# Kernel tuning notes

Hardware: AMD Instinct MI355X
Metric: run time of the kernel (lower is better)

## Reference

```python
import jax, jax.numpy as jnp
import numpy as np

B, DIM = 64, 1024

def setup_inputs() -> dict:
    key = jax.random.key(0)
    ks = jax.random.split(key, 16)
    d = {
        'x': jax.random.normal(ks[0], (B, DIM), jnp.float32),
        'C': jax.random.normal(ks[1], (B, DIM, DIM), jnp.float32) * 0.02,
        'n': jax.random.normal(ks[2], (B, DIM), jnp.float32),
        'm': jax.random.normal(ks[3], (B, DIM), jnp.float32),
    }
    s = 1.0 / np.sqrt(DIM)
    names = ['q', 'k', 'v', 'i', 'f', 'o']
    for j, nm in enumerate(names):
        d['W' + nm] = jax.random.uniform(ks[4 + 2 * j], (DIM, DIM), jnp.float32, -s, s)
        d['b' + nm] = jax.random.uniform(ks[5 + 2 * j], (DIM,), jnp.float32, -s, s)
    return d

def _lin(x, W, b):
    # torch nn.Linear: x @ W.T + b
    return x @ W.T + b

def reference(x, C, n, m, Wq, bq, Wk, bk, Wv, bv, Wi, bi, Wf, bf, Wo, bo):
    q = _lin(x, Wq, bq)                      # [B, D]
    k = _lin(x, Wk, bk) / jnp.sqrt(jnp.float32(DIM))
    v = _lin(x, Wv, bv)
    i_t = _lin(x, Wi, bi)
    f_t = _lin(x, Wf, bf)
    m_new = jnp.maximum(f_t + m, i_t)        # [B, D]
    i = jnp.exp(i_t - m_new)                 # [B, D]
    f = jnp.exp(f_t + m - m_new)             # [B, D]
    # rank-1 covariance update: C_new[b,r,c] = f[b,r]*C[b,r,c] + i[b,r]*v[b,r]*k[b,c]
    C_new = f[:, :, None] * C + (i * v)[:, :, None] * k[:, None, :]
    n_new = f * n + i * k
    h = jax.nn.sigmoid(_lin(x, Wo, bo)) * jnp.einsum('brc,bc->br', C_new, q)
    return (h, C_new, n_new, m_new)
```

## Files before the change

kernel.cpp:

```cpp
#include <hip/hip_runtime.h>
#include <math.h>

#define BATCH 64
#define DIM 1024
#define NROW (BATCH * DIM)
#define OFF_H 0
#define OFF_C 65536
#define OFF_N (65536 + 67108864)
#define OFF_M (OFF_N + 65536)

typedef float f4 __attribute__((ext_vector_type(4)));


__global__ __launch_bounds__(256) void gemm6(
    const float* __restrict__ x,
    const float* __restrict__ Wq, const float* __restrict__ bq,
    const float* __restrict__ Wk, const float* __restrict__ bk,
    const float* __restrict__ Wv, const float* __restrict__ bv,
    const float* __restrict__ Wi, const float* __restrict__ bi,
    const float* __restrict__ Wf, const float* __restrict__ bf,
    const float* __restrict__ Wo, const float* __restrict__ bo,
    float* __restrict__ pre)
{
    __shared__ float xs[64][64];
    __shared__ float wl[64][17];

    const int bx = blockIdx.x;
    const int g = bx >> 6;
    const int j0 = (bx & 63) * 16;
    const float* W; const float* bias;
    switch (g) {
        case 0: W = Wq; bias = bq; break;
        case 1: W = Wk; bias = bk; break;
        case 2: W = Wv; bias = bv; break;
        case 3: W = Wi; bias = bi; break;
        case 4: W = Wf; bias = bf; break;
        default: W = Wo; bias = bo; break;
    }

    const int tid = threadIdx.x;
    const int tj = tid & 15;
    const int tb = tid >> 4;

    const int xb = tid & 63;
    const int xc = tid >> 6;
    const int wj = tid >> 4;
    const int wk = tid & 15;

    float acc[4] = {0.f, 0.f, 0.f, 0.f};

    for (int k0 = 0; k0 < DIM; k0 += 64) {
        #pragma unroll
        for (int it = 0; it < 4; ++it) {
            const int cq = xc * 4 + it;
            float4 v = *reinterpret_cast<const float4*>(&x[xb * DIM + k0 + cq * 4]);
            xs[cq * 4 + 0][xb] = v.x;
            xs[cq * 4 + 1][xb] = v.y;
            xs[cq * 4 + 2][xb] = v.z;
            xs[cq * 4 + 3][xb] = v.w;
        }
        {
            float4 v = *reinterpret_cast<const float4*>(&W[(j0 + wj) * DIM + k0 + wk * 4]);
            wl[wk * 4 + 0][wj] = v.x;
            wl[wk * 4 + 1][wj] = v.y;
            wl[wk * 4 + 2][wj] = v.z;
            wl[wk * 4 + 3][wj] = v.w;
        }
        __syncthreads();
        #pragma unroll
        for (int kk = 0; kk < 64; ++kk) {
            float4 xv = *reinterpret_cast<const float4*>(&xs[kk][tb * 4]);
            float wv = wl[kk][tj];
            acc[0] += xv.x * wv;
            acc[1] += xv.y * wv;
            acc[2] += xv.z * wv;
            acc[3] += xv.w * wv;
        }
        __syncthreads();
    }

    const float bv_ = bias[j0 + tj];
    const int jcol = j0 + tj;
    #pragma unroll
    for (int e = 0; e < 4; ++e) {
        const int b = tb * 4 + e;
        pre[g * NROW + b * DIM + jcol] = acc[e] + bv_;
    }
}

__global__ __launch_bounds__(256) void cupdate(
    const float* __restrict__ C,
    const float* __restrict__ n_in, const float* __restrict__ m_in,
    const float* __restrict__ ws,
    float* __restrict__ out)
{
    const int row  = blockIdx.x * 4 + (threadIdx.x >> 6);
    const int lane = threadIdx.x & 63;
    const int b    = row >> 10;

    const float ip  = ws[3 * NROW + row];
    const float fp_ = ws[4 * NROW + row];
    const float op  = ws[5 * NROW + row];
    const float vp  = ws[2 * NROW + row];
    const float mo  = m_in[row];

    const float mn  = fmaxf(fp_ + mo, ip);
    const float iex = expf(ip - mn);
    const float fex = expf(fp_ + mo - mn);
    const float so  = 1.f / (1.f + expf(-op));
    const float iv  = iex * vp;

    const f4* k4 = reinterpret_cast<const f4*>(ws + 1 * NROW + b * DIM);
    const f4* q4 = reinterpret_cast<const f4*>(ws + 0 * NROW + b * DIM);
    const f4* C4 = reinterpret_cast<const f4*>(C) + (size_t)row * 256;
    f4*       O4 = reinterpret_cast<f4*>(out + OFF_C) + (size_t)row * 256;

    const float ksc = iv * 0.03125f;

    float dot = 0.f;
    #pragma unroll
    for (int i = 0; i < 4; ++i) {
        const int c4 = lane + 64 * i;
        f4 cv = __builtin_nontemporal_load(&C4[c4]);
        f4 kv = k4[c4];
        f4 qv = q4[c4];
        f4 cn = fex * cv + ksc * kv;
        __builtin_nontemporal_store(cn, &O4[c4]);
        f4 pr = cn * qv;
        dot += pr.x + pr.y + pr.z + pr.w;
    }
    #pragma unroll
    for (int off = 32; off > 0; off >>= 1)
        dot += __shfl_xor(dot, off, 64);

    if (lane == 0) {
        out[OFF_H + row] = so * dot;
        const float no   = n_in[row];
        const float kp_r = ws[1 * NROW + row] * 0.03125f;
        out[OFF_N + row] = fex * no + iex * kp_r;
        out[OFF_M + row] = mn;
    }
}

extern "C" void kernel_launch(void* const* d_in, const int* in_sizes, int n_in,
                              void* d_out, int out_size, void* d_ws, size_t ws_size,
                              hipStream_t stream) {
    const float* x = (const float*)d_in[0];
    const float* C = (const float*)d_in[1];
    const float* n = (const float*)d_in[2];
    const float* m = (const float*)d_in[3];
    float* ws  = (float*)d_ws;
    float* out = (float*)d_out;

    gemm6<<<384, 256, 0, stream>>>(
        x,
        (const float*)d_in[4],  (const float*)d_in[5],
        (const float*)d_in[6],  (const float*)d_in[7],
        (const float*)d_in[8],  (const float*)d_in[9],
        (const float*)d_in[10], (const float*)d_in[11],
        (const float*)d_in[12], (const float*)d_in[13],
        (const float*)d_in[14], (const float*)d_in[15],
        ws);
    cupdate<<<NROW / 4, 256, 0, stream>>>(C, n, m, ws, out);
}
```

Measured before the change: 135.6 us.

## Replace FP32 shared-memory projection GEMM with bf16 MFMA direct-from-global

The six-way projection GEMM now converts x and W rows to bf16 in registers and accumulates with 16x16x32 bf16 MFMA instructions, dropping the shared-memory tiling and barriers. Each wave computes a 16x16 output tile, with two independent accumulators to hide MFMA latency. The goal is to shorten the GEMM stage, which runs before the bandwidth-bound covariance update. The cost is reduced input precision (bf16), which may shift results against an fp32 reference, plus repeated uncached global reads of x across blocks.

```diff
diff --git a/kernel.cpp b/kernel.cpp
--- a/kernel.cpp
+++ b/kernel.cpp
@@ -1,4 +1,5 @@
 #include <hip/hip_runtime.h>
+#include <hip/hip_bf16.h>
 #include <math.h>
 
 #define BATCH 64
@@ -9,83 +10,76 @@
 #define OFF_N (65536 + 67108864)
 #define OFF_M (OFF_N + 65536)
 
-typedef float f4 __attribute__((ext_vector_type(4)));
+typedef float f4     __attribute__((ext_vector_type(4)));
+typedef float f32x4  __attribute__((ext_vector_type(4)));
+typedef short bf16x8 __attribute__((ext_vector_type(8)));
 
 
-__global__ __launch_bounds__(256) void gemm6(
+__device__ inline short f2bf(float v) {
+    __hip_bfloat16 h = __float2bfloat16(v);
+    short s;
+    __builtin_memcpy(&s, &h, 2);
+    return s;
+}
+
+__device__ inline bf16x8 load_bf8(const float* __restrict__ p) {
+    f4 a = *reinterpret_cast<const f4*>(p);
+    f4 b = *reinterpret_cast<const f4*>(p + 4);
+    bf16x8 r;
+    r[0] = f2bf(a.x); r[1] = f2bf(a.y); r[2] = f2bf(a.z); r[3] = f2bf(a.w);
+    r[4] = f2bf(b.x); r[5] = f2bf(b.y); r[6] = f2bf(b.z); r[7] = f2bf(b.w);
+    return r;
+}
+
+__global__ __launch_bounds__(256) void gemm6_mfma(
     const float* __restrict__ x,
     const float* __restrict__ Wq, const float* __restrict__ bq,
     const float* __restrict__ Wk, const float* __restrict__ bk,
     const float* __restrict__ Wv, const float* __restrict__ bv,
     const float* __restrict__ Wi, const float* __restrict__ bi,
-    const float* __restrict__ Wf, const float* __restrict__ bf,
+    const float* __restrict__ Wf, const float* __restrict__ bf_,
     const float* __restrict__ Wo, const float* __restrict__ bo,
     float* __restrict__ pre)
 {
-    __shared__ float xs[64][64];
-    __shared__ float wl[64][17];
-
     const int bx = blockIdx.x;
-    const int g = bx >> 6;
-    const int j0 = (bx & 63) * 16;
+    const int g  = bx >> 6;
+    const int j0 = (bx & 63) << 4;
     const float* W; const float* bias;
     switch (g) {
         case 0: W = Wq; bias = bq; break;
         case 1: W = Wk; bias = bk; break;
         case 2: W = Wv; bias = bv; break;
         case 3: W = Wi; bias = bi; break;
-        case 4: W = Wf; bias = bf; break;
+        case 4: W = Wf; bias = bf_; break;
         default: W = Wo; bias = bo; break;
     }
 
-    const int tid = threadIdx.x;
-    const int tj = tid & 15;
-    const int tb = tid >> 4;
+    const int wave = threadIdx.x >> 6;
+    const int lane = threadIdx.x & 63;
+    const int l15  = lane & 15;
+    const int kq   = lane >> 4;
 
-    const int xb = tid & 63;
-    const int xc = tid >> 6;
-    const int wj = tid >> 4;
-    const int wk = tid & 15;
+    const float* xrow = x + (size_t)(wave * 16 + l15) * DIM + kq * 8;
+    const float* wrow = W + (size_t)(j0 + l15) * DIM + kq * 8;
 
-    float acc[4] = {0.f, 0.f, 0.f, 0.f};
+    f32x4 acc0 = {0.f, 0.f, 0.f, 0.f};
+    f32x4 acc1 = {0.f, 0.f, 0.f, 0.f};
+    #pragma unroll 4
+    for (int kt = 0; kt < 32; kt += 2) {
+        bf16x8 a0 = load_bf8(xrow + kt * 32);
+        bf16x8 b0 = load_bf8(wrow + kt * 32);
+        bf16x8 a1 = load_bf8(xrow + kt * 32 + 32);
+        bf16x8 b1 = load_bf8(wrow + kt * 32 + 32);
+        acc0 = __builtin_amdgcn_mfma_f32_16x16x32_bf16(a0, b0, acc0, 0, 0, 0);
+        acc1 = __builtin_amdgcn_mfma_f32_16x16x32_bf16(a1, b1, acc1, 0, 0, 0);
+    }
+    acc0 += acc1;
 
-    for (int k0 = 0; k0 < DIM; k0 += 64) {
-        #pragma unroll
-        for (int it = 0; it < 4; ++it) {
-            const int cq = xc * 4 + it;
-            float4 v = *reinterpret_cast<const float4*>(&x[xb * DIM + k0 + cq * 4]);
-            xs[cq * 4 + 0][xb] = v.x;
-            xs[cq * 4 + 1][xb] = v.y;
-            xs[cq * 4 + 2][xb] = v.z;
-            xs[cq * 4 + 3][xb] = v.w;
-        }
-        {
-            float4 v = *reinterpret_cast<const float4*>(&W[(j0 + wj) * DIM + k0 + wk * 4]);
-            wl[wk * 4 + 0][wj] = v.x;
-            wl[wk * 4 + 1][wj] = v.y;
-            wl[wk * 4 + 2][wj] = v.z;
-            wl[wk * 4 + 3][wj] = v.w;
-        }
-        __syncthreads();
-        #pragma unroll
-        for (int kk = 0; kk < 64; ++kk) {
-            float4 xv = *reinterpret_cast<const float4*>(&xs[kk][tb * 4]);
-            float wv = wl[kk][tj];
-            acc[0] += xv.x * wv;
-            acc[1] += xv.y * wv;
-            acc[2] += xv.z * wv;
-            acc[3] += xv.w * wv;
-        }
-        __syncthreads();
-    }
-
-    const float bv_ = bias[j0 + tj];
-    const int jcol = j0 + tj;
+    const float bv_ = bias[j0 + l15];
+    float* dst = pre + (size_t)g * NROW + (size_t)(wave * 16 + kq * 4) * DIM + j0 + l15;
     #pragma unroll
-    for (int e = 0; e < 4; ++e) {
-        const int b = tb * 4 + e;
-        pre[g * NROW + b * DIM + jcol] = acc[e] + bv_;
-    }
+    for (int r = 0; r < 4; ++r)
+        dst[(size_t)r * DIM] = acc0[r] + bv_;
 }
 
 __global__ __launch_bounds__(256) void cupdate(
@@ -152,7 +146,7 @@
     float* ws  = (float*)d_ws;
     float* out = (float*)d_out;
 
-    gemm6<<<384, 256, 0, stream>>>(
+    gemm6_mfma<<<384, 256, 0, stream>>>(
         x,
         (const float*)d_in[4],  (const float*)d_in[5],
         (const float*)d_in[6],  (const float*)d_in[7],
```

Result: faster. 129.6 us (-4.4%).
